# Performance work log

Measured on AMD Instinct MI355X. Metric: run time of the kernel, lower is better.

Reference implementation:

```python
import jax, jax.numpy as jnp
import numpy as np

B, L, H, W_MAX, N_CLASSES = 32, 2048, 768, 512, 16


def setup_inputs() -> dict:
    key = jax.random.key(0)
    k_enc, k_len, k_w1, k_w2 = jax.random.split(key, 4)
    encoder_output = jax.random.normal(k_enc, (B, L, H), dtype=jnp.float32)
    # Ragged word spans: word lengths in [1, 8], consecutive spans via exclusive cumsum.
    lengths = jax.random.randint(k_len, (B, W_MAX), 1, 9)
    ends = jnp.cumsum(lengths, axis=1).astype(jnp.int32)
    starts = (ends - lengths).astype(jnp.int32)
    # Spans running past L become invalid (mask=0), matching the original's guard.
    W1 = jax.random.normal(k_w1, (H, H // 2), dtype=jnp.float32) * 0.02
    b1 = jnp.zeros((H // 2,), dtype=jnp.float32)
    W2 = jax.random.normal(k_w2, (H // 2, N_CLASSES), dtype=jnp.float32) * 0.02
    b2 = jnp.zeros((N_CLASSES,), dtype=jnp.float32)
    return {"encoder_output": encoder_output, "starts": starts, "ends": ends,
            "W1": W1, "b1": b1, "W2": W2, "b2": b2}


def reference(encoder_output, starts, ends, W1, b1, W2, b2):
    Bq, Lq, Hq = encoder_output.shape
    # Validity guard identical to original: s < L and e <= L and s < e
    valid = (starts < Lq) & (ends <= Lq) & (starts < ends)          # (B, W)
    mask = valid.astype(jnp.float32)
    # Prefix sums over sequence dim (zero-prepended): (B, L+1, H)
    csum = jnp.concatenate(
        [jnp.zeros((Bq, 1, Hq), encoder_output.dtype),
         jnp.cumsum(encoder_output, axis=1)], axis=1)
    s_idx = jnp.clip(starts, 0, Lq)[:, :, None]                      # (B, W, 1)
    e_idx = jnp.clip(ends, 0, Lq)[:, :, None]
    span_sum = (jnp.take_along_axis(csum, e_idx, axis=1)
                - jnp.take_along_axis(csum, s_idx, axis=1))          # (B, W, H)
    counts = jnp.maximum(ends - starts, 1).astype(encoder_output.dtype)[:, :, None]
    pooled = jnp.where(valid[:, :, None], span_sum / counts, 0.0)    # (B, W, H)
    # MLP head (dropout is identity in eval mode); torch GELU default = exact erf
    h = jax.nn.gelu(pooled @ W1 + b1, approximate=False)
    logits = h @ W2 + b2                                             # (B, W, n_classes)
    return logits, mask
```

## Files before the change

kernel.cpp:

```cpp
#include <hip/hip_runtime.h>
#include <hip/hip_bf16.h>

#define B_   32
#define L_   2048
#define H_   768
#define W_   512
#define NC_  16
#define HH_  384
#define NWORDS (B_ * W_)
#define NLOGITS (NWORDS * NC_)

#define BM    32
#define LDA   776
#define LDH   388

typedef __attribute__((ext_vector_type(8))) __bf16 bf16x8;
typedef __attribute__((ext_vector_type(4))) float floatx4;

static __device__ __forceinline__ unsigned short f2bf(float x) {
    union { float f; unsigned u; } v; v.f = x;
    unsigned r = v.u + 0x7FFF + ((v.u >> 16) & 1);
    return (unsigned short)(r >> 16);
}

__global__ __launch_bounds__(256) void k_convert_w1(const float* __restrict__ W1,
                                                    unsigned short* __restrict__ w1t) {
    __shared__ unsigned short tile[64][65];
    const int k0 = blockIdx.x * 64;
    const int n0 = blockIdx.y * 64;
    const int tx = threadIdx.x & 63;
    const int ty = threadIdx.x >> 6;
    #pragma unroll
    for (int r = 0; r < 64; r += 4)
        tile[r + ty][tx] = f2bf(W1[(size_t)(k0 + r + ty) * HH_ + n0 + tx]);
    __syncthreads();
    #pragma unroll
    for (int r = 0; r < 64; r += 4)
        w1t[(size_t)(n0 + r + ty) * H_ + k0 + tx] = tile[tx][r + ty];
}

__global__ __launch_bounds__(512, 4) void k_fused(
    const float* __restrict__ enc,
    const int* __restrict__ starts,
    const int* __restrict__ ends,
    const unsigned short* __restrict__ w1t,
    const float* __restrict__ b1,
    const float* __restrict__ W2,
    const float* __restrict__ b2,
    float* __restrict__ out)
{
    __shared__ float smem[BM * LDH];
    unsigned short* sA = (unsigned short*)smem;

    const int tid  = threadIdx.x;
    const int wave = tid >> 6, lane = tid & 63;
    const int m0 = blockIdx.x * BM;
    const int b  = m0 >> 9;

    #pragma unroll
    for (int wi = 0; wi < 4; ++wi) {
        const int wloc = wave * 4 + wi;
        const int gw   = m0 + wloc;
        const int s = starts[gw], e = ends[gw];
        const int len = e - s;
        const bool valid = (s < L_) && (e <= L_);
        floatx4 a0 = {0.f,0.f,0.f,0.f}, a1 = a0, a2 = a0;
        if (valid) {
            const float* rowbase = enc + (size_t)b * (L_ * H_);
            const float inv = 1.0f / (float)len;
            floatx4 v0[8], v1[8], v2[8];
            #pragma unroll
            for (int r = 0; r < 8; ++r) {
                int row = s + r; row = (row < L_) ? row : (L_ - 1);
                const floatx4* p = (const floatx4*)(rowbase + (size_t)row * H_) + lane;
                v0[r] = p[0]; v1[r] = p[64]; v2[r] = p[128];
            }
            #pragma unroll
            for (int r = 0; r < 8; ++r) {
                const float wr = (r < len) ? inv : 0.f;
                a0 += wr * v0[r]; a1 += wr * v1[r]; a2 += wr * v2[r];
            }
        }
        unsigned short* dst = sA + wloc * LDA + lane * 4;
        ushort4 o;
        o.x=f2bf(a0[0]); o.y=f2bf(a0[1]); o.z=f2bf(a0[2]); o.w=f2bf(a0[3]); *(ushort4*)(dst)       = o;
        o.x=f2bf(a1[0]); o.y=f2bf(a1[1]); o.z=f2bf(a1[2]); o.w=f2bf(a1[3]); *(ushort4*)(dst + 256) = o;
        o.x=f2bf(a2[0]); o.y=f2bf(a2[1]); o.z=f2bf(a2[2]); o.w=f2bf(a2[3]); *(ushort4*)(dst + 512) = o;
        if (lane == 0) out[NLOGITS + gw] = valid ? 1.0f : 0.0f;
    }
    __syncthreads();

    const int lr = lane & 15, lk = lane >> 4;
    floatx4 acc[2][3];
    #pragma unroll
    for (int i = 0; i < 2; ++i)
        #pragma unroll
        for (int j = 0; j < 3; ++j) acc[i][j] = {0.f,0.f,0.f,0.f};

    const unsigned short* sa0 = sA + lr * LDA + lk * 8;
    const unsigned short* bp0 = w1t + (size_t)(wave * 48 +  0 + lr) * H_ + lk * 8;
    const unsigned short* bp1 = w1t + (size_t)(wave * 48 + 16 + lr) * H_ + lk * 8;
    const unsigned short* bp2 = w1t + (size_t)(wave * 48 + 32 + lr) * H_ + lk * 8;

    #pragma unroll
    for (int kk = 0; kk < 24; ++kk) {
        const int ko = kk * 32;
        bf16x8 af0 = *(const bf16x8*)(sa0 + ko);
        bf16x8 af1 = *(const bf16x8*)(sa0 + 16 * LDA + ko);
        bf16x8 bf0 = *(const bf16x8*)(bp0 + ko);
        bf16x8 bf1 = *(const bf16x8*)(bp1 + ko);
        bf16x8 bf2 = *(const bf16x8*)(bp2 + ko);
        acc[0][0] = __builtin_amdgcn_mfma_f32_16x16x32_bf16(af0, bf0, acc[0][0], 0, 0, 0);
        acc[1][0] = __builtin_amdgcn_mfma_f32_16x16x32_bf16(af1, bf0, acc[1][0], 0, 0, 0);
        acc[0][1] = __builtin_amdgcn_mfma_f32_16x16x32_bf16(af0, bf1, acc[0][1], 0, 0, 0);
        acc[1][1] = __builtin_amdgcn_mfma_f32_16x16x32_bf16(af1, bf1, acc[1][1], 0, 0, 0);
        acc[0][2] = __builtin_amdgcn_mfma_f32_16x16x32_bf16(af0, bf2, acc[0][2], 0, 0, 0);
        acc[1][2] = __builtin_amdgcn_mfma_f32_16x16x32_bf16(af1, bf2, acc[1][2], 0, 0, 0);
    }
    __syncthreads();

    #pragma unroll
    for (int ni = 0; ni < 3; ++ni) {
        const int col = wave * 48 + ni * 16 + lr;
        const float bias = b1[col];
        #pragma unroll
        for (int mi = 0; mi < 2; ++mi) {
            #pragma unroll
            for (int r = 0; r < 4; ++r) {
                const int row = mi * 16 + lk * 4 + r;
                const float x = acc[mi][ni][r] + bias;
                const float g = 0.5f * x * (1.0f + erff(x * 0.70710678118654752f));
                smem[row * LDH + col] = g;
            }
        }
    }
    __syncthreads();

    const int r = tid >> 4;
    const int c = tid & 15;
    const float* hrow = smem + r * LDH;
    float s0 = 0.f, s1 = 0.f, s2 = 0.f, s3 = 0.f;
    #pragma unroll 4
    for (int k = 0; k < HH_; k += 4) {
        const float4 hv = *(const float4*)(hrow + k);
        s0 += hv.x * W2[(k + 0) * NC_ + c];
        s1 += hv.y * W2[(k + 1) * NC_ + c];
        s2 += hv.z * W2[(k + 2) * NC_ + c];
        s3 += hv.w * W2[(k + 3) * NC_ + c];
    }
    out[(size_t)(m0 + r) * NC_ + c] = b2[c] + ((s0 + s1) + (s2 + s3));
}

extern "C" void kernel_launch(void* const* d_in, const int* in_sizes, int n_in,
                              void* d_out, int out_size, void* d_ws, size_t ws_size,
                              hipStream_t stream) {
    const float* enc    = (const float*)d_in[0];
    const int*   starts = (const int*)d_in[1];
    const int*   ends   = (const int*)d_in[2];
    const float* W1     = (const float*)d_in[3];
    const float* b1     = (const float*)d_in[4];
    const float* W2     = (const float*)d_in[5];
    const float* b2     = (const float*)d_in[6];
    float* out = (float*)d_out;

    unsigned short* w1t = (unsigned short*)d_ws;

    hipLaunchKernelGGL(k_convert_w1, dim3(H_ / 64, HH_ / 64), dim3(256), 0, stream, W1, w1t);
    hipLaunchKernelGGL(k_fused, dim3(NWORDS / BM), dim3(512), 0, stream,
                       enc, starts, ends, w1t, b1, W2, b2, out);
}
```

Before: 333.6 us.

## Split fused pool+MLP kernel into separate pool, GEMM1 and GEMM2 kernels

Breaks the single fused kernel into three launches: span pooling writes bf16 pooled rows to workspace, a GEMM1 kernel with 64-row tiles and K-tiled LDS staging applies bias and GELU and writes fp32 h, and a GEMM2 kernel stages h and W2 in LDS. The aim is to decouple the memory-bound gather from the MFMA GEMM, get higher occupancy and larger GEMM tiles, and read W2 from LDS instead of global memory. In exchange it adds global round-trips for the pooled activations (about 25 MB) and h (about 25 MB), plus extra launch overhead. Pool loads now clamp to the span length, so rows past the span are not fetched.

```diff
diff --git a/kernel.cpp b/kernel.cpp
--- a/kernel.cpp
+++ b/kernel.cpp
@@ -9,10 +9,6 @@
 #define HH_  384
 #define NWORDS (B_ * W_)
 #define NLOGITS (NWORDS * NC_)
-
-#define BM    32
-#define LDA   776
-#define LDH   388
 
 typedef __attribute__((ext_vector_type(8))) __bf16 bf16x8;
 typedef __attribute__((ext_vector_type(4))) float floatx4;
@@ -39,114 +35,133 @@
         w1t[(size_t)(n0 + r + ty) * H_ + k0 + tx] = tile[tx][r + ty];
 }
 
-__global__ __launch_bounds__(512, 4) void k_fused(
-    const float* __restrict__ enc,
-    const int* __restrict__ starts,
-    const int* __restrict__ ends,
-    const unsigned short* __restrict__ w1t,
-    const float* __restrict__ b1,
-    const float* __restrict__ W2,
-    const float* __restrict__ b2,
-    float* __restrict__ out)
-{
-    __shared__ float smem[BM * LDH];
-    unsigned short* sA = (unsigned short*)smem;
+__global__ __launch_bounds__(256) void k_pool(const float* __restrict__ enc,
+                                              const int* __restrict__ starts,
+                                              const int* __restrict__ ends,
+                                              unsigned short* __restrict__ pooled,
+                                              float* __restrict__ mask) {
+    const int wave = threadIdx.x >> 6, lane = threadIdx.x & 63;
+    const int gw = blockIdx.x * 4 + wave;
+    const int s = starts[gw], e = ends[gw];
+    const int len = e - s;
+    const bool valid = (s < L_) && (e <= L_) && (s < e);
+    floatx4 a0 = {0.f,0.f,0.f,0.f}, a1 = a0, a2 = a0;
+    if (valid) {
+        const int b = gw >> 9;
+        const float* base = enc + ((size_t)b * L_ + s) * H_ + lane * 4;
+        floatx4 v0[8], v1[8], v2[8];
+        #pragma unroll
+        for (int r = 0; r < 8; ++r) {
+            const int ro = ((r < len) ? r : (len - 1)) * H_;
+            const floatx4* p = (const floatx4*)(base + ro);
+            v0[r] = p[0]; v1[r] = p[64]; v2[r] = p[128];
+        }
+        __builtin_amdgcn_sched_barrier(0);
+        const float inv = 1.0f / (float)len;
+        #pragma unroll
+        for (int r = 0; r < 8; ++r) {
+            const float wr = (r < len) ? inv : 0.f;
+            a0 += wr * v0[r]; a1 += wr * v1[r]; a2 += wr * v2[r];
+        }
+    }
+    unsigned short* dst = pooled + (size_t)gw * H_ + lane * 4;
+    ushort4 o;
+    o.x=f2bf(a0[0]); o.y=f2bf(a0[1]); o.z=f2bf(a0[2]); o.w=f2bf(a0[3]); *(ushort4*)(dst)       = o;
+    o.x=f2bf(a1[0]); o.y=f2bf(a1[1]); o.z=f2bf(a1[2]); o.w=f2bf(a1[3]); *(ushort4*)(dst + 256) = o;
+    o.x=f2bf(a2[0]); o.y=f2bf(a2[1]); o.z=f2bf(a2[2]); o.w=f2bf(a2[3]); *(ushort4*)(dst + 512) = o;
+    if (lane == 0) mask[gw] = valid ? 1.0f : 0.0f;
+}
 
+#define G1_LDA 72
+__global__ __launch_bounds__(512) void k_gemm1(const unsigned short* __restrict__ pooled,
+                                               const unsigned short* __restrict__ w1t,
+                                               const float* __restrict__ b1,
+                                               float* __restrict__ h) {
+    __shared__ unsigned short sA[64 * G1_LDA];
     const int tid  = threadIdx.x;
     const int wave = tid >> 6, lane = tid & 63;
-    const int m0 = blockIdx.x * BM;
-    const int b  = m0 >> 9;
+    const int wm = wave >> 2, wn = wave & 3;
+    const int lr = lane & 15, lk = lane >> 4;
+    const int m0 = blockIdx.x * 64;
 
-    #pragma unroll
-    for (int wi = 0; wi < 4; ++wi) {
-        const int wloc = wave * 4 + wi;
-        const int gw   = m0 + wloc;
-        const int s = starts[gw], e = ends[gw];
-        const int len = e - s;
-        const bool valid = (s < L_) && (e <= L_);
-        floatx4 a0 = {0.f,0.f,0.f,0.f}, a1 = a0, a2 = a0;
-        if (valid) {
-            const float* rowbase = enc + (size_t)b * (L_ * H_);
-            const float inv = 1.0f / (float)len;
-            floatx4 v0[8], v1[8], v2[8];
-            #pragma unroll
-            for (int r = 0; r < 8; ++r) {
-                int row = s + r; row = (row < L_) ? row : (L_ - 1);
-                const floatx4* p = (const floatx4*)(rowbase + (size_t)row * H_) + lane;
-                v0[r] = p[0]; v1[r] = p[64]; v2[r] = p[128];
-            }
-            #pragma unroll
-            for (int r = 0; r < 8; ++r) {
-                const float wr = (r < len) ? inv : 0.f;
-                a0 += wr * v0[r]; a1 += wr * v1[r]; a2 += wr * v2[r];
-            }
-        }
-        unsigned short* dst = sA + wloc * LDA + lane * 4;
-        ushort4 o;
-        o.x=f2bf(a0[0]); o.y=f2bf(a0[1]); o.z=f2bf(a0[2]); o.w=f2bf(a0[3]); *(ushort4*)(dst)       = o;
-        o.x=f2bf(a1[0]); o.y=f2bf(a1[1]); o.z=f2bf(a1[2]); o.w=f2bf(a1[3]); *(ushort4*)(dst + 256) = o;
-        o.x=f2bf(a2[0]); o.y=f2bf(a2[1]); o.z=f2bf(a2[2]); o.w=f2bf(a2[3]); *(ushort4*)(dst + 512) = o;
-        if (lane == 0) out[NLOGITS + gw] = valid ? 1.0f : 0.0f;
-    }
-    __syncthreads();
-
-    const int lr = lane & 15, lk = lane >> 4;
-    floatx4 acc[2][3];
+    floatx4 acc[2][6];
     #pragma unroll
     for (int i = 0; i < 2; ++i)
         #pragma unroll
-        for (int j = 0; j < 3; ++j) acc[i][j] = {0.f,0.f,0.f,0.f};
+        for (int j = 0; j < 6; ++j) acc[i][j] = {0.f,0.f,0.f,0.f};
 
-    const unsigned short* sa0 = sA + lr * LDA + lk * 8;
-    const unsigned short* bp0 = w1t + (size_t)(wave * 48 +  0 + lr) * H_ + lk * 8;
-    const unsigned short* bp1 = w1t + (size_t)(wave * 48 + 16 + lr) * H_ + lk * 8;
-    const unsigned short* bp2 = w1t + (size_t)(wave * 48 + 32 + lr) * H_ + lk * 8;
+    const int srow = tid >> 3;
+    const int sseg = (tid & 7) * 8;
+    const unsigned short* bbase = w1t + (size_t)(wn * 96 + lr) * H_ + lk * 8;
+
+    for (int kt = 0; kt < 12; ++kt) {
+        const int k0 = kt * 64;
+        bf16x8 av = *(const bf16x8*)(pooled + (size_t)(m0 + srow) * H_ + k0 + sseg);
+        if (kt) __syncthreads();
+        *(bf16x8*)(sA + srow * G1_LDA + sseg) = av;
+        __syncthreads();
+        #pragma unroll
+        for (int kk = 0; kk < 2; ++kk) {
+            bf16x8 af0 = *(const bf16x8*)(sA + (wm * 32 +  0 + lr) * G1_LDA + kk * 32 + lk * 8);
+            bf16x8 af1 = *(const bf16x8*)(sA + (wm * 32 + 16 + lr) * G1_LDA + kk * 32 + lk * 8);
+            bf16x8 bf[6];
+            #pragma unroll
+            for (int ni = 0; ni < 6; ++ni)
+                bf[ni] = *(const bf16x8*)(bbase + (size_t)ni * 16 * H_ + k0 + kk * 32);
+            #pragma unroll
+            for (int ni = 0; ni < 6; ++ni) {
+                acc[0][ni] = __builtin_amdgcn_mfma_f32_16x16x32_bf16(af0, bf[ni], acc[0][ni], 0, 0, 0);
+                acc[1][ni] = __builtin_amdgcn_mfma_f32_16x16x32_bf16(af1, bf[ni], acc[1][ni], 0, 0, 0);
+            }
+        }
+    }
 
     #pragma unroll
-    for (int kk = 0; kk < 24; ++kk) {
-        const int ko = kk * 32;
-        bf16x8 af0 = *(const bf16x8*)(sa0 + ko);
-        bf16x8 af1 = *(const bf16x8*)(sa0 + 16 * LDA + ko);
-        bf16x8 bf0 = *(const bf16x8*)(bp0 + ko);
-        bf16x8 bf1 = *(const bf16x8*)(bp1 + ko);
-        bf16x8 bf2 = *(const bf16x8*)(bp2 + ko);
-        acc[0][0] = __builtin_amdgcn_mfma_f32_16x16x32_bf16(af0, bf0, acc[0][0], 0, 0, 0);
-        acc[1][0] = __builtin_amdgcn_mfma_f32_16x16x32_bf16(af1, bf0, acc[1][0], 0, 0, 0);
-        acc[0][1] = __builtin_amdgcn_mfma_f32_16x16x32_bf16(af0, bf1, acc[0][1], 0, 0, 0);
-        acc[1][1] = __builtin_amdgcn_mfma_f32_16x16x32_bf16(af1, bf1, acc[1][1], 0, 0, 0);
-        acc[0][2] = __builtin_amdgcn_mfma_f32_16x16x32_bf16(af0, bf2, acc[0][2], 0, 0, 0);
-        acc[1][2] = __builtin_amdgcn_mfma_f32_16x16x32_bf16(af1, bf2, acc[1][2], 0, 0, 0);
-    }
-    __syncthreads();
-
-    #pragma unroll
-    for (int ni = 0; ni < 3; ++ni) {
-        const int col = wave * 48 + ni * 16 + lr;
+    for (int ni = 0; ni < 6; ++ni) {
+        const int col = wn * 96 + ni * 16 + lr;
         const float bias = b1[col];
         #pragma unroll
         for (int mi = 0; mi < 2; ++mi) {
             #pragma unroll
             for (int r = 0; r < 4; ++r) {
-                const int row = mi * 16 + lk * 4 + r;
+                const int row = wm * 32 + mi * 16 + lk * 4 + r;
                 const float x = acc[mi][ni][r] + bias;
                 const float g = 0.5f * x * (1.0f + erff(x * 0.70710678118654752f));
-                smem[row * LDH + col] = g;
+                h[(size_t)(m0 + row) * HH_ + col] = g;
             }
         }
     }
+}
+
+__global__ __launch_bounds__(256) void k_gemm2(const float* __restrict__ h,
+                                               const float* __restrict__ W2,
+                                               const float* __restrict__ b2,
+                                               float* __restrict__ out) {
+    __shared__ float sh[16 * 388];
+    __shared__ float sw[HH_ * NC_];
+    const int tid = threadIdx.x;
+    const int m0 = blockIdx.x * 16;
+    const int r = tid >> 4, cseg = (tid & 15) * 4;
+    #pragma unroll
+    for (int j = 0; j < 6; ++j)
+        *(float4*)(sh + r * 388 + cseg + j * 64) =
+            *(const float4*)(h + (size_t)(m0 + r) * HH_ + cseg + j * 64);
+    #pragma unroll
+    for (int j = 0; j < 6; ++j) {
+        const int idx = tid * 4 + j * 1024;
+        *(float4*)(sw + idx) = *(const float4*)(W2 + idx);
+    }
     __syncthreads();
-
-    const int r = tid >> 4;
     const int c = tid & 15;
-    const float* hrow = smem + r * LDH;
+    const float* hrow = sh + r * 388;
     float s0 = 0.f, s1 = 0.f, s2 = 0.f, s3 = 0.f;
-    #pragma unroll 4
+    #pragma unroll 8
     for (int k = 0; k < HH_; k += 4) {
         const float4 hv = *(const float4*)(hrow + k);
-        s0 += hv.x * W2[(k + 0) * NC_ + c];
-        s1 += hv.y * W2[(k + 1) * NC_ + c];
-        s2 += hv.z * W2[(k + 2) * NC_ + c];
-        s3 += hv.w * W2[(k + 3) * NC_ + c];
+        s0 += hv.x * sw[(k + 0) * NC_ + c];
+        s1 += hv.y * sw[(k + 1) * NC_ + c];
+        s2 += hv.z * sw[(k + 2) * NC_ + c];
+        s3 += hv.w * sw[(k + 3) * NC_ + c];
     }
     out[(size_t)(m0 + r) * NC_ + c] = b2[c] + ((s0 + s1) + (s2 + s3));
 }
@@ -163,9 +178,13 @@
     const float* b2     = (const float*)d_in[6];
     float* out = (float*)d_out;
 
-    unsigned short* w1t = (unsigned short*)d_ws;
+    unsigned short* w1t    = (unsigned short*)d_ws;
+    unsigned short* pooled = w1t + (size_t)HH_ * H_;
+    float*          hbuf   = (float*)(pooled + (size_t)NWORDS * H_);
+    float*          mask   = out + NLOGITS;
 
     hipLaunchKernelGGL(k_convert_w1, dim3(H_ / 64, HH_ / 64), dim3(256), 0, stream, W1, w1t);
-    hipLaunchKernelGGL(k_fused, dim3(NWORDS / BM), dim3(512), 0, stream,
-                       enc, starts, ends, w1t, b1, W2, b2, out);
+    hipLaunchKernelGGL(k_pool, dim3(NWORDS / 4), dim3(256), 0, stream, enc, starts, ends, pooled, mask);
+    hipLaunchKernelGGL(k_gemm1, dim3(NWORDS / 64), dim3(512), 0, stream, pooled, w1t, b1, hbuf);
+    hipLaunchKernelGGL(k_gemm2, dim3(NWORDS / 16), dim3(256), 0, stream, hbuf, W2, b2, out);
 }
```

Result: slower. 353.1 us (+5.8%).

## Split fused kernel into separate pooling and MLP kernels via bf16 workspace

Applied to the files above, without the earlier changes.

Splits the fused pooling+MLP kernel into a pooling kernel with one wave per word, which writes bf16 pooled rows to a workspace, and an MLP kernel that stages those rows into LDS. It also caches W2 in shared memory for the second GEMV and clamps row reads to the span length rather than to L. The aim is higher memory-level parallelism for the bandwidth-bound ragged gather, at the cost of an extra kernel launch and a round trip of the pooled activations through global memory.

```diff
diff --git a/kernel.cpp b/kernel.cpp
--- a/kernel.cpp
+++ b/kernel.cpp
@@ -9,10 +9,6 @@
 #define HH_  384
 #define NWORDS (B_ * W_)
 #define NLOGITS (NWORDS * NC_)
-
-#define BM    32
-#define LDA   776
-#define LDH   388
 
 typedef __attribute__((ext_vector_type(8))) __bf16 bf16x8;
 typedef __attribute__((ext_vector_type(4))) float floatx4;
@@ -39,54 +35,73 @@
         w1t[(size_t)(n0 + r + ty) * H_ + k0 + tx] = tile[tx][r + ty];
 }
 
-__global__ __launch_bounds__(512, 4) void k_fused(
-    const float* __restrict__ enc,
-    const int* __restrict__ starts,
-    const int* __restrict__ ends,
-    const unsigned short* __restrict__ w1t,
-    const float* __restrict__ b1,
-    const float* __restrict__ W2,
-    const float* __restrict__ b2,
-    float* __restrict__ out)
-{
+__global__ __launch_bounds__(256) void k_pool(const float* __restrict__ enc,
+                                              const int* __restrict__ starts,
+                                              const int* __restrict__ ends,
+                                              unsigned short* __restrict__ pooled,
+                                              float* __restrict__ mask) {
+    const int wave = threadIdx.x >> 6, lane = threadIdx.x & 63;
+    const int gw = blockIdx.x * 4 + wave;
+    const int s = starts[gw], e = ends[gw];
+    const int len = e - s;
+    const bool valid = (s < L_) && (e <= L_) && (s < e);
+    floatx4 a0 = {0.f,0.f,0.f,0.f}, a1 = a0, a2 = a0;
+    if (valid) {
+        const int b = gw >> 9;
+        const float* base = enc + ((size_t)b * L_ + s) * H_ + lane * 4;
+        floatx4 v0[8], v1[8], v2[8];
+        #pragma unroll
+        for (int r = 0; r < 8; ++r) {
+            const int ro = ((r < len) ? r : (len - 1)) * H_;
+            const floatx4* p = (const floatx4*)(base + ro);
+            v0[r] = p[0]; v1[r] = p[64]; v2[r] = p[128];
+        }
+        __builtin_amdgcn_sched_barrier(0);
+        const float inv = 1.0f / (float)len;
+        #pragma unroll
+        for (int r = 0; r < 8; ++r) {
+            const float wr = (r < len) ? inv : 0.f;
+            a0 += wr * v0[r]; a1 += wr * v1[r]; a2 += wr * v2[r];
+        }
+    }
+    unsigned short* dst = pooled + (size_t)gw * H_ + lane * 4;
+    ushort4 o;
+    o.x=f2bf(a0[0]); o.y=f2bf(a0[1]); o.z=f2bf(a0[2]); o.w=f2bf(a0[3]); *(ushort4*)(dst)       = o;
+    o.x=f2bf(a1[0]); o.y=f2bf(a1[1]); o.z=f2bf(a1[2]); o.w=f2bf(a1[3]); *(ushort4*)(dst + 256) = o;
+    o.x=f2bf(a2[0]); o.y=f2bf(a2[1]); o.z=f2bf(a2[2]); o.w=f2bf(a2[3]); *(ushort4*)(dst + 512) = o;
+    if (lane == 0) mask[gw] = valid ? 1.0f : 0.0f;
+}
+
+#define BM   32
+#define LDA  776
+#define LDH  388
+__global__ __launch_bounds__(512) void k_mlp(const unsigned short* __restrict__ pooled,
+                                             const unsigned short* __restrict__ w1t,
+                                             const float* __restrict__ b1,
+                                             const float* __restrict__ W2,
+                                             const float* __restrict__ b2,
+                                             float* __restrict__ out) {
     __shared__ float smem[BM * LDH];
+    __shared__ float swW2[HH_ * NC_];
     unsigned short* sA = (unsigned short*)smem;
 
     const int tid  = threadIdx.x;
     const int wave = tid >> 6, lane = tid & 63;
     const int m0 = blockIdx.x * BM;
-    const int b  = m0 >> 9;
 
     #pragma unroll
-    for (int wi = 0; wi < 4; ++wi) {
-        const int wloc = wave * 4 + wi;
-        const int gw   = m0 + wloc;
-        const int s = starts[gw], e = ends[gw];
-        const int len = e - s;
-        const bool valid = (s < L_) && (e <= L_);
-        floatx4 a0 = {0.f,0.f,0.f,0.f}, a1 = a0, a2 = a0;
-        if (valid) {
-            const float* rowbase = enc + (size_t)b * (L_ * H_);
-            const float inv = 1.0f / (float)len;
-            floatx4 v0[8], v1[8], v2[8];
-            #pragma unroll
-            for (int r = 0; r < 8; ++r) {
-                int row = s + r; row = (row < L_) ? row : (L_ - 1);
-                const floatx4* p = (const floatx4*)(rowbase + (size_t)row * H_) + lane;
-                v0[r] = p[0]; v1[r] = p[64]; v2[r] = p[128];
-            }
-            #pragma unroll
-            for (int r = 0; r < 8; ++r) {
-                const float wr = (r < len) ? inv : 0.f;
-                a0 += wr * v0[r]; a1 += wr * v1[r]; a2 += wr * v2[r];
-            }
+    for (int j = 0; j < 3; ++j)
+        *(float4*)(swW2 + tid * 4 + j * 2048) = *(const float4*)(W2 + tid * 4 + j * 2048);
+
+    {
+        const int row = tid >> 4, t16 = tid & 15;
+        const unsigned short* src = pooled + (size_t)(m0 + row) * H_;
+        unsigned short* dstrow = sA + row * LDA;
+        #pragma unroll
+        for (int j = 0; j < 6; ++j) {
+            const int off = (t16 + 16 * j) * 8;
+            *(bf16x8*)(dstrow + off) = *(const bf16x8*)(src + off);
         }
-        unsigned short* dst = sA + wloc * LDA + lane * 4;
-        ushort4 o;
-        o.x=f2bf(a0[0]); o.y=f2bf(a0[1]); o.z=f2bf(a0[2]); o.w=f2bf(a0[3]); *(ushort4*)(dst)       = o;
-        o.x=f2bf(a1[0]); o.y=f2bf(a1[1]); o.z=f2bf(a1[2]); o.w=f2bf(a1[3]); *(ushort4*)(dst + 256) = o;
-        o.x=f2bf(a2[0]); o.y=f2bf(a2[1]); o.z=f2bf(a2[2]); o.w=f2bf(a2[3]); *(ushort4*)(dst + 512) = o;
-        if (lane == 0) out[NLOGITS + gw] = valid ? 1.0f : 0.0f;
     }
     __syncthreads();
 
@@ -140,13 +155,13 @@
     const int c = tid & 15;
     const float* hrow = smem + r * LDH;
     float s0 = 0.f, s1 = 0.f, s2 = 0.f, s3 = 0.f;
-    #pragma unroll 4
+    #pragma unroll 8
     for (int k = 0; k < HH_; k += 4) {
         const float4 hv = *(const float4*)(hrow + k);
-        s0 += hv.x * W2[(k + 0) * NC_ + c];
-        s1 += hv.y * W2[(k + 1) * NC_ + c];
-        s2 += hv.z * W2[(k + 2) * NC_ + c];
-        s3 += hv.w * W2[(k + 3) * NC_ + c];
+        s0 += hv.x * swW2[(k + 0) * NC_ + c];
+        s1 += hv.y * swW2[(k + 1) * NC_ + c];
+        s2 += hv.z * swW2[(k + 2) * NC_ + c];
+        s3 += hv.w * swW2[(k + 3) * NC_ + c];
     }
     out[(size_t)(m0 + r) * NC_ + c] = b2[c] + ((s0 + s1) + (s2 + s3));
 }
@@ -163,9 +178,11 @@
     const float* b2     = (const float*)d_in[6];
     float* out = (float*)d_out;
 
-    unsigned short* w1t = (unsigned short*)d_ws;
+    unsigned short* w1t    = (unsigned short*)d_ws;
+    unsigned short* pooled = w1t + (size_t)HH_ * H_;
+    float*          mask   = out + NLOGITS;
 
     hipLaunchKernelGGL(k_convert_w1, dim3(H_ / 64, HH_ / 64), dim3(256), 0, stream, W1, w1t);
-    hipLaunchKernelGGL(k_fused, dim3(NWORDS / BM), dim3(512), 0, stream,
-                       enc, starts, ends, w1t, b1, W2, b2, out);
+    hipLaunchKernelGGL(k_pool, dim3(NWORDS / 4), dim3(256), 0, stream, enc, starts, ends, pooled, mask);
+    hipLaunchKernelGGL(k_mlp, dim3(NWORDS / BM), dim3(512), 0, stream, pooled, w1t, b1, W2, b2, out);
 }
```

New measurement: 335.5 us. Within noise of the previous version (+0.6%).
